# Kernel tuning notes

Hardware: AMD Instinct MI355X
Metric: run time of the kernel (lower is better)

Reference implementation:

```python
import jax, jax.numpy as jnp
import numpy as np

BN_EPS = 1e-5


def _fps(xyz, n_centers):
    """Furthest point sampling. xyz: (B,N,3) -> idx (B,n_centers) int32.
    Deterministic start at index 0 (torch version uses randint start)."""
    B, N, _ = xyz.shape
    batch_ar = jnp.arange(B)

    def step(carry, _):
        distances, farthest = carry  # (B,N), (B,)
        center = xyz[batch_ar, farthest]  # (B,3)
        d = jnp.sum((xyz - center[:, None, :]) ** 2, axis=-1)  # (B,N)
        distances = jnp.minimum(distances, d)
        new_far = jnp.argmax(distances, axis=-1)
        return (distances, new_far), farthest

    init = (jnp.full((B, N), jnp.inf, dtype=xyz.dtype),
            jnp.zeros((B,), dtype=jnp.int32))
    _, idxs = jax.lax.scan(step, init, None, length=n_centers)  # (n_centers, B)
    return idxs.T  # (B, n_centers)


def _knn_group(xyz, centers, k):
    """xyz:(B,N,3), centers:(B,M,3) -> patches (B,M,k,3) center-relative."""
    # (B,M,N) squared distances
    dists = jnp.sum((centers[:, :, None, :] - xyz[:, None, :, :]) ** 2, axis=-1)
    _, idx = jax.lax.top_k(-dists, k)  # (B,M,k) smallest distances
    # gather neighbor coords: (B,M,k,3)
    patches = jnp.take_along_axis(xyz[:, None, :, :], idx[..., None], axis=2)
    return patches - centers[:, :, None, :]


def _bn_eval(x, gamma, beta):
    # BatchNorm1d in eval mode: running_mean=0, running_var=1
    return x * (gamma / jnp.sqrt(1.0 + BN_EPS)) + beta


def _mini_pointnet(patches, W1, b1, g1, bt1, W2, b2, g2, bt2, W3, b3, g3, bt3):
    B, M, k, C = patches.shape
    x = patches.reshape(B * M * k, C)
    x = jax.nn.relu(_bn_eval(x @ W1 + b1, g1, bt1))
    x = jax.nn.relu(_bn_eval(x @ W2 + b2, g2, bt2))
    x = jax.nn.relu(_bn_eval(x @ W3 + b3, g3, bt3))
    x = x.reshape(B * M, k, -1).max(axis=1)
    return x.reshape(B, M, -1)


def setup_inputs() -> dict:
    key = jax.random.key(0)
    ks = jax.random.split(key, 8)
    B, N = 16, 16384
    embed = 256

    def lin(kk, fan_in, fan_out):
        bound = 1.0 / np.sqrt(fan_in)
        k1, k2 = jax.random.split(kk)
        W = jax.random.uniform(k1, (fan_in, fan_out), jnp.float32, -bound, bound)
        b = jax.random.uniform(k2, (fan_out,), jnp.float32, -bound, bound)
        return W, b

    W1, b1 = lin(ks[1], 3, 64)
    W2, b2 = lin(ks[2], 64, 128)
    W3, b3 = lin(ks[3], 128, embed)
    return {
        "xyz": jax.random.normal(ks[0], (B, N, 3), jnp.float32),
        "W1": W1, "b1": b1, "g1": jnp.ones((64,)), "bt1": jnp.zeros((64,)),
        "W2": W2, "b2": b2, "g2": jnp.ones((128,)), "bt2": jnp.zeros((128,)),
        "W3": W3, "b3": b3, "g3": jnp.ones((embed,)), "bt3": jnp.zeros((embed,)),
        "n_centers": 256,
        "k": 32,
    }


def reference(xyz, W1, b1, g1, bt1, W2, b2, g2, bt2, W3, b3, g3, bt3,
              n_centers, k):
    center_idx = _fps(xyz, n_centers)  # (B, M)
    centers = jnp.take_along_axis(xyz, center_idx[..., None], axis=1)  # (B,M,3)
    patches = _knn_group(xyz, centers, k)  # (B,M,k,3)
    tokens = _mini_pointnet(patches, W1, b1, g1, bt1, W2, b2, g2, bt2,
                            W3, b3, g3, bt3)
    return tokens, centers
```

## Files before the change

### kernel.cpp

```cpp
#include <hip/hip_runtime.h>

constexpr int B   = 16;
constexpr int N   = 16384;
constexpr int M   = 256;
constexpr int K   = 32;
constexpr int EMB = 256;

__device__ __forceinline__ float sqdist(float px, float py, float pz,
                                        float cx, float cy, float cz) {
  float dx = __fsub_rn(px, cx);
  float dy = __fsub_rn(py, cy);
  float dz = __fsub_rn(pz, cz);
  return __fadd_rn(__fadd_rn(__fmul_rn(dx, dx), __fmul_rn(dy, dy)),
                   __fmul_rn(dz, dz));
}

constexpr int FT = 512;
constexpr int FP = N / FT;
constexpr int FW = FT / 64;
static_assert(FT == 512 && FP == 32, "macro expansion assumes 512x32");

#define FPS_REP(X) X(0) X(1) X(2) X(3) X(4) X(5) X(6) X(7) X(8) X(9) \
  X(10) X(11) X(12) X(13) X(14) X(15) X(16) X(17) X(18) X(19) \
  X(20) X(21) X(22) X(23) X(24) X(25) X(26) X(27) X(28) X(29) X(30) X(31)

__global__ __launch_bounds__(FT)
__attribute__((amdgpu_waves_per_eu(2, 2)))
void fps_kernel(const float* __restrict__ xyz, float* __restrict__ centers) {
  const int b = blockIdx.x;
  const int tid = threadIdx.x;
  const float* base = xyz + (size_t)b * N * 3;

#define FPS_DECL(i) float px##i, py##i, pz##i, ds##i;
  FPS_REP(FPS_DECL)
#undef FPS_DECL

#define FPS_LOAD(i) { const int n = tid + (i) * FT;      \
    px##i = base[n * 3 + 0];                              \
    py##i = base[n * 3 + 1];                              \
    pz##i = base[n * 3 + 2];                              \
    ds##i = __builtin_inff(); }
  FPS_REP(FPS_LOAD)
#undef FPS_LOAD

#define FPS_PIN(i) asm volatile("" : "+v"(px##i), "+v"(py##i), "+v"(pz##i));
  FPS_REP(FPS_PIN)
#undef FPS_PIN

  __shared__ float s_pv[2][FW];
  __shared__ int s_pn[2][FW];

  float cx = base[0], cy = base[1], cz = base[2];

  for (int it = 0; it < M; ++it) {
    if (tid == 0) {
      float* co = centers + ((size_t)b * M + it) * 3;
      co[0] = cx; co[1] = cy; co[2] = cz;
    }
    const int p = it & 1;

    float bv = -1.0f;
    int bj = 0;
#define FPS_UPD(i) {                                       \
    float dx = __fsub_rn(px##i, cx);                       \
    float dy = __fsub_rn(py##i, cy);                       \
    float dz = __fsub_rn(pz##i, cz);                       \
    float dd = __fadd_rn(__fadd_rn(__fmul_rn(dx, dx),      \
                                   __fmul_rn(dy, dy)),     \
                         __fmul_rn(dz, dz));               \
    float nd = fminf(ds##i, dd);                           \
    ds##i = nd;                                            \
    bool g = nd > bv;                                      \
    bv = g ? nd : bv;                                      \
    bj = g ? (i) : bj; }
    FPS_REP(FPS_UPD)
#undef FPS_UPD
    int bn = (bj << 9) + tid;

#pragma unroll
    for (int mm = 32; mm >= 1; mm >>= 1) {
      float ov = __shfl_xor(bv, mm, 64);
      int on = __shfl_xor(bn, mm, 64);
      if (ov > bv || (ov == bv && on < bn)) { bv = ov; bn = on; }
    }
    if ((tid & 63) == 0) {
      s_pv[p][tid >> 6] = bv;
      s_pn[p][tid >> 6] = bn;
    }
    __syncthreads();

    float v = s_pv[p][0];
    int n = s_pn[p][0];
#pragma unroll
    for (int w = 1; w < FW; ++w) {
      float ov = s_pv[p][w];
      int on = s_pn[p][w];
      if (ov > v || (ov == v && on < n)) { v = ov; n = on; }
    }
    cx = base[(size_t)n * 3 + 0];
    cy = base[(size_t)n * 3 + 1];
    cz = base[(size_t)n * 3 + 2];
  }
}

constexpr int KT = 256;
constexpr int CAP = 512;
constexpr int NBUCKET = 1024;

__global__ __launch_bounds__(KT) void knn_kernel(
    const float* __restrict__ xyz, const float* __restrict__ centers,
    float* __restrict__ patches) {
  const int blk = blockIdx.x;
  const int b = blk >> 8;
  const int tid = threadIdx.x;
  const float* base = xyz + (size_t)b * N * 3;

  __shared__ int hist[NBUCKET];
  __shared__ unsigned cb[CAP];
  __shared__ int ci[CAP];
  __shared__ int s_nin, s_ncand, s_tb;
  __shared__ int s_wsum[KT / 64];
  __shared__ float s_cc[3];

  if (tid == 0) {
    const float* c = centers + (size_t)blk * 3;
    s_cc[0] = c[0]; s_cc[1] = c[1]; s_cc[2] = c[2];
    s_nin = 0; s_ncand = 0;
  }
  for (int i = tid; i < NBUCKET; i += KT) hist[i] = 0;
  __syncthreads();

  const float cx = s_cc[0], cy = s_cc[1], cz = s_cc[2];

  for (int n = tid; n < N; n += KT) {
    float d = sqdist(base[n * 3], base[n * 3 + 1], base[n * 3 + 2], cx, cy, cz);
    atomicAdd(&hist[__float_as_uint(d) >> 21], 1);
  }
  __syncthreads();

  int h0[4];
  int loc = 0;
#pragma unroll
  for (int i = 0; i < 4; ++i) { h0[i] = hist[tid * 4 + i]; loc += h0[i]; }
  int lane = tid & 63, wid = tid >> 6;
  int scan = loc;
  for (int off = 1; off < 64; off <<= 1) {
    int o = __shfl_up(scan, off, 64);
    if (lane >= off) scan += o;
  }
  if (lane == 63) s_wsum[wid] = scan;
  __syncthreads();
  int woff = 0;
  for (int w = 0; w < wid; ++w) woff += s_wsum[w];
  int c0 = woff + scan - loc;
#pragma unroll
  for (int i = 0; i < 4; ++i) {
    int c1 = c0 + h0[i];
    if (c0 < K && c1 >= K) s_tb = tid * 4 + i;
    c0 = c1;
  }
  __syncthreads();
  const int tb = s_tb;
  const unsigned lo = (unsigned)tb << 21;
  const unsigned hi = (unsigned)(tb + 1) << 21;

  for (int n = tid; n < N; n += KT) {
    float x = base[n * 3], y = base[n * 3 + 1], z = base[n * 3 + 2];
    float d = sqdist(x, y, z, cx, cy, cz);
    unsigned bits = __float_as_uint(d);
    if (bits < lo) {
      int pos = atomicAdd(&s_nin, 1);
      float* p = patches + ((size_t)blk * K + pos) * 3;
      p[0] = __fsub_rn(x, cx); p[1] = __fsub_rn(y, cy); p[2] = __fsub_rn(z, cz);
    } else if (bits < hi) {
      int q = atomicAdd(&s_ncand, 1);
      if (q < CAP) { cb[q] = bits; ci[q] = n; }
    }
  }
  __syncthreads();

  const int nin = s_nin;
  const int ncand = min(s_ncand, CAP);
  const int nsel = K - nin;
  for (int j = tid; j < ncand; j += KT) {
    unsigned bj = cb[j];
    int ij = ci[j];
    int rank = 0;
    for (int i2 = 0; i2 < ncand; ++i2) {
      unsigned bv = cb[i2];
      int iv = ci[i2];
      rank += (bv < bj || (bv == bj && iv < ij)) ? 1 : 0;
    }
    if (rank < nsel) {
      float x = base[ij * 3], y = base[ij * 3 + 1], z = base[ij * 3 + 2];
      float* p = patches + ((size_t)blk * K + nin + rank) * 3;
      p[0] = __fsub_rn(x, cx); p[1] = __fsub_rn(y, cy); p[2] = __fsub_rn(z, cz);
    }
  }
}

constexpr int MT = 128;

__global__ __launch_bounds__(MT) void mlp_kernel(
    const float* __restrict__ patches,
    const float* __restrict__ W1, const float* __restrict__ b1,
    const float* __restrict__ g1, const float* __restrict__ bt1,
    const float* __restrict__ W2, const float* __restrict__ b2,
    const float* __restrict__ g2, const float* __restrict__ bt2,
    const float* __restrict__ W3, const float* __restrict__ b3,
    const float* __restrict__ g3, const float* __restrict__ bt3,
    float* __restrict__ tokens) {
  const int pm = blockIdx.x;
  const int tid = threadIdx.x;
  __shared__ float xs[3][K];
  __shared__ float h1s[64 * K];
  __shared__ float h2s[128 * K];
  __shared__ float pms[2][EMB];

  const float* patch = patches + (size_t)pm * (K * 3);
  if (tid < 96) xs[tid % 3][tid / 3] = patch[tid];
  __syncthreads();

  const int cg = tid & 63;
  const int half = tid >> 6;
  const int pt0 = half * 16;
  const float rs = 1.0f / sqrtf(1.0f + 1e-5f);

  {
    const int c = cg;
    const float w0 = W1[c], w1 = W1[64 + c], w2 = W1[128 + c];
    const float bb = b1[c];
    const float sc = g1[c] * rs, be = bt1[c];
    float o[16];
#pragma unroll
    for (int p = 0; p < 16; ++p) {
      int pt = pt0 + p;
      float a = xs[0][pt] * w0 + xs[1][pt] * w1 + xs[2][pt] * w2 + bb;
      o[p] = fmaxf(a * sc + be, 0.0f);
    }
    const int so = (c & 7) << 2;
#pragma unroll
    for (int p4 = 0; p4 < 16; p4 += 4) {
      *(float4*)&h1s[c * K + ((pt0 + p4) ^ so)] =
          make_float4(o[p4], o[p4 + 1], o[p4 + 2], o[p4 + 3]);
    }
  }
  __syncthreads();

  {
    const int c = cg * 2;
    float acc0[16], acc1[16];
    const float bb0 = b2[c], bb1 = b2[c + 1];
#pragma unroll
    for (int p = 0; p < 16; ++p) { acc0[p] = bb0; acc1[p] = bb1; }
    for (int k = 0; k < 64; ++k) {
      const float2 w = *(const float2*)(W2 + k * 128 + c);
      const int so = (k & 7) << 2;
      float4 x0 = *(const float4*)&h1s[k * K + ((pt0 + 0) ^ so)];
      float4 x1 = *(const float4*)&h1s[k * K + ((pt0 + 4) ^ so)];
      float4 x2 = *(const float4*)&h1s[k * K + ((pt0 + 8) ^ so)];
      float4 x3 = *(const float4*)&h1s[k * K + ((pt0 + 12) ^ so)];
      float xv[16] = {x0.x, x0.y, x0.z, x0.w, x1.x, x1.y, x1.z, x1.w,
                      x2.x, x2.y, x2.z, x2.w, x3.x, x3.y, x3.z, x3.w};
#pragma unroll
      for (int p = 0; p < 16; ++p) {
        acc0[p] += xv[p] * w.x;
        acc1[p] += xv[p] * w.y;
      }
    }
    const float sc0 = g2[c] * rs, be0 = bt2[c];
    const float sc1 = g2[c + 1] * rs, be1 = bt2[c + 1];
    float o0[16], o1[16];
#pragma unroll
    for (int p = 0; p < 16; ++p) {
      o0[p] = fmaxf(acc0[p] * sc0 + be0, 0.0f);
      o1[p] = fmaxf(acc1[p] * sc1 + be1, 0.0f);
    }
    const int soa = (c & 7) << 2, sob = ((c + 1) & 7) << 2;
#pragma unroll
    for (int p4 = 0; p4 < 16; p4 += 4) {
      *(float4*)&h2s[c * K + ((pt0 + p4) ^ soa)] =
          make_float4(o0[p4], o0[p4 + 1], o0[p4 + 2], o0[p4 + 3]);
      *(float4*)&h2s[(c + 1) * K + ((pt0 + p4) ^ sob)] =
          make_float4(o1[p4], o1[p4 + 1], o1[p4 + 2], o1[p4 + 3]);
    }
  }
  __syncthreads();

  {
    const int c = cg * 4;
    float acc[4][16];
#pragma unroll
    for (int i = 0; i < 4; ++i) {
      const float bb = b3[c + i];
#pragma unroll
      for (int p = 0; p < 16; ++p) acc[i][p] = bb;
    }
    for (int k = 0; k < 128; ++k) {
      const float4 w = *(const float4*)(W3 + (size_t)k * 256 + c);
      const int so = (k & 7) << 2;
      float4 x0 = *(const float4*)&h2s[k * K + ((pt0 + 0) ^ so)];
      float4 x1 = *(const float4*)&h2s[k * K + ((pt0 + 4) ^ so)];
      float4 x2 = *(const float4*)&h2s[k * K + ((pt0 + 8) ^ so)];
      float4 x3 = *(const float4*)&h2s[k * K + ((pt0 + 12) ^ so)];
      float xv[16] = {x0.x, x0.y, x0.z, x0.w, x1.x, x1.y, x1.z, x1.w,
                      x2.x, x2.y, x2.z, x2.w, x3.x, x3.y, x3.z, x3.w};
#pragma unroll
      for (int p = 0; p < 16; ++p) {
        acc[0][p] += xv[p] * w.x;
        acc[1][p] += xv[p] * w.y;
        acc[2][p] += xv[p] * w.z;
        acc[3][p] += xv[p] * w.w;
      }
    }
#pragma unroll
    for (int i = 0; i < 4; ++i) {
      const float sc = g3[c + i] * rs, be = bt3[c + i];
      float mx = 0.0f;
#pragma unroll
      for (int p = 0; p < 16; ++p)
        mx = fmaxf(mx, fmaxf(acc[i][p] * sc + be, 0.0f));
      pms[half][c + i] = mx;
    }
  }
  __syncthreads();

  {
    const int c2 = tid * 2;
    float* to = tokens + (size_t)pm * EMB;
    to[c2] = fmaxf(pms[0][c2], pms[1][c2]);
    to[c2 + 1] = fmaxf(pms[0][c2 + 1], pms[1][c2 + 1]);
  }
}

extern "C" void kernel_launch(void* const* d_in, const int* in_sizes, int n_in,
                              void* d_out, int out_size, void* d_ws,
                              size_t ws_size, hipStream_t stream) {
  const float* xyz = (const float*)d_in[0];
  const float* W1 = (const float*)d_in[1];
  const float* b1 = (const float*)d_in[2];
  const float* g1 = (const float*)d_in[3];
  const float* bt1 = (const float*)d_in[4];
  const float* W2 = (const float*)d_in[5];
  const float* b2 = (const float*)d_in[6];
  const float* g2 = (const float*)d_in[7];
  const float* bt2 = (const float*)d_in[8];
  const float* W3 = (const float*)d_in[9];
  const float* b3 = (const float*)d_in[10];
  const float* g3 = (const float*)d_in[11];
  const float* bt3 = (const float*)d_in[12];

  float* tokens = (float*)d_out;
  float* centers = tokens + (size_t)B * M * EMB;
  float* patches = (float*)d_ws;

  fps_kernel<<<B, FT, 0, stream>>>(xyz, centers);
  knn_kernel<<<B * M, KT, 0, stream>>>(xyz, centers, patches);
  mlp_kernel<<<B * M, MT, 0, stream>>>(patches, W1, b1, g1, bt1, W2, b2, g2,
                                       bt2, W3, b3, g3, bt3, tokens);
}
```

Before: 802.0 us.

## Widen FPS block to 1024 threads and spill running distances to LDS

The furthest-point-sampling kernel now uses 1024 threads per batch, so each thread owns 16 points instead of 32. Running min-distances for 15 of those slots move from registers to shared memory, and only the last slot stays in a register. This lowers register pressure enough to fit 4 waves per EU, giving more parallelism on the serial 256-iteration loop. The cost is an LDS read and write per point per iteration and a wider block-level reduction (16 waves instead of 8).

```diff
diff --git a/kernel.cpp b/kernel.cpp
--- a/kernel.cpp
+++ b/kernel.cpp
@@ -15,40 +15,46 @@
                    __fmul_rn(dz, dz));
 }
 
-constexpr int FT = 512;
-constexpr int FP = N / FT;
+constexpr int FT = 1024;
+constexpr int FPP = N / FT;
 constexpr int FW = FT / 64;
-static_assert(FT == 512 && FP == 32, "macro expansion assumes 512x32");
-
-#define FPS_REP(X) X(0) X(1) X(2) X(3) X(4) X(5) X(6) X(7) X(8) X(9) \
-  X(10) X(11) X(12) X(13) X(14) X(15) X(16) X(17) X(18) X(19) \
-  X(20) X(21) X(22) X(23) X(24) X(25) X(26) X(27) X(28) X(29) X(30) X(31)
-
-__global__ __launch_bounds__(FT)
-__attribute__((amdgpu_waves_per_eu(2, 2)))
+
+#define FPS_REP16(X) X(0) X(1) X(2) X(3) X(4) X(5) X(6) X(7) X(8) X(9) \
+  X(10) X(11) X(12) X(13) X(14) X(15)
+#define FPS_REP15(X) X(0) X(1) X(2) X(3) X(4) X(5) X(6) X(7) X(8) X(9) \
+  X(10) X(11) X(12) X(13) X(14)
+
+__global__ __launch_bounds__(FT, 4)
+__attribute__((amdgpu_waves_per_eu(4, 4)))
 void fps_kernel(const float* __restrict__ xyz, float* __restrict__ centers) {
   const int b = blockIdx.x;
   const int tid = threadIdx.x;
   const float* base = xyz + (size_t)b * N * 3;
 
-#define FPS_DECL(i) float px##i, py##i, pz##i, ds##i;
-  FPS_REP(FPS_DECL)
+  __shared__ float s_dist[15 * FT];
+  __shared__ float s_pv[2][FW];
+  __shared__ int s_pn[2][FW];
+
+#define FPS_DECL(i) float px##i, py##i, pz##i;
+  FPS_REP16(FPS_DECL)
 #undef FPS_DECL
+  float ds15;
 
 #define FPS_LOAD(i) { const int n = tid + (i) * FT;      \
     px##i = base[n * 3 + 0];                              \
     py##i = base[n * 3 + 1];                              \
-    pz##i = base[n * 3 + 2];                              \
-    ds##i = __builtin_inff(); }
-  FPS_REP(FPS_LOAD)
+    pz##i = base[n * 3 + 2]; }
+  FPS_REP16(FPS_LOAD)
 #undef FPS_LOAD
 
+#define FPS_INIT(i) s_dist[tid + (i) * FT] = __builtin_inff();
+  FPS_REP15(FPS_INIT)
+#undef FPS_INIT
+  ds15 = __builtin_inff();
+
 #define FPS_PIN(i) asm volatile("" : "+v"(px##i), "+v"(py##i), "+v"(pz##i));
-  FPS_REP(FPS_PIN)
+  FPS_REP16(FPS_PIN)
 #undef FPS_PIN
-
-  __shared__ float s_pv[2][FW];
-  __shared__ int s_pn[2][FW];
 
   float cx = base[0], cy = base[1], cz = base[2];
 
@@ -68,14 +74,27 @@
     float dd = __fadd_rn(__fadd_rn(__fmul_rn(dx, dx),      \
                                    __fmul_rn(dy, dy)),     \
                          __fmul_rn(dz, dz));               \
-    float nd = fminf(ds##i, dd);                           \
-    ds##i = nd;                                            \
+    float od = s_dist[tid + (i) * FT];                     \
+    float nd = fminf(od, dd);                              \
+    s_dist[tid + (i) * FT] = nd;                           \
     bool g = nd > bv;                                      \
     bv = g ? nd : bv;                                      \
     bj = g ? (i) : bj; }
-    FPS_REP(FPS_UPD)
+    FPS_REP15(FPS_UPD)
 #undef FPS_UPD
-    int bn = (bj << 9) + tid;
+    {
+      float dx = __fsub_rn(px15, cx);
+      float dy = __fsub_rn(py15, cy);
+      float dz = __fsub_rn(pz15, cz);
+      float dd = __fadd_rn(__fadd_rn(__fmul_rn(dx, dx), __fmul_rn(dy, dy)),
+                           __fmul_rn(dz, dz));
+      float nd = fminf(ds15, dd);
+      ds15 = nd;
+      bool g = nd > bv;
+      bv = g ? nd : bv;
+      bj = g ? 15 : bj;
+    }
+    int bn = (bj << 10) + tid;
 
 #pragma unroll
     for (int mm = 32; mm >= 1; mm >>= 1) {
```

New measurement: 1.013 ms. 1.26x slower.
